# Optimization experiments

Hardware: AMD Instinct MI355X
Metric: run time of the kernel (lower is better)

## Reference

```python
import jax, jax.numpy as jnp
import numpy as np

N_NODES = 100000
N_EDGES = 600000
D = 128
BN_EPS = 1e-5


def setup_inputs() -> dict:
    key = jax.random.key(0)
    k1, k2, k3 = jax.random.split(key, 3)
    x = jax.random.normal(k1, (N_NODES, D), dtype=jnp.float32)
    edge_index = jax.random.randint(k2, (2, N_EDGES), 0, N_NODES, dtype=jnp.int64)
    # Linear(in=D, out=D): kaiming-uniform-ish init
    W = jax.random.normal(k3, (D, D), dtype=jnp.float32) / np.sqrt(D)
    b = jnp.zeros((D,), dtype=jnp.float32)
    eps_gin = jnp.zeros((), dtype=jnp.float32)  # train_eps=True, init 0
    gamma = jnp.ones((D,), dtype=jnp.float32)
    beta = jnp.zeros((D,), dtype=jnp.float32)
    return {"x": x, "edge_index": edge_index, "W": W, "b": b,
            "eps_gin": eps_gin, "gamma": gamma, "beta": beta}


def reference(x, edge_index, W, b, eps_gin, gamma, beta):
    src, dst = edge_index[0], edge_index[1]
    # GIN aggregation: sum of source features into destination nodes
    agg = jax.ops.segment_sum(x[src], dst, num_segments=N_NODES)  # [N, D]
    h = (1.0 + eps_gin) * x + agg
    # MLP([D, D]) == single Linear (PyG plain_last)
    h = jnp.einsum('nd,df->nf', h, W.T) + b  # torch Linear: h @ W^T + b
    # BatchNorm1d in training mode (batch stats, biased variance)
    mean = jnp.mean(h, axis=0)
    var = jnp.mean((h - mean) ** 2, axis=0)
    h = (h - mean) * jax.lax.rsqrt(var + BN_EPS) * gamma + beta
    h = jax.nn.relu(h)
    # residual
    return h + x
```

## Files before the change

### kernel.cpp

```cpp
#include <hip/hip_runtime.h>
#include <hip/hip_bf16.h>

#define N_NODES 100000
#define N_EDGES 600000
#define D 128
#define BN_EPS 1e-5f
#define CAP 40
#define NSLOTS 2048

typedef __bf16 bf16x8 __attribute__((ext_vector_type(8)));
typedef float floatx4 __attribute__((ext_vector_type(4)));
typedef unsigned short ushortx8 __attribute__((ext_vector_type(8)));

__device__ __forceinline__ unsigned short f2bf(float f) {
    union { float f; unsigned u; } v; v.f = f;
    unsigned u = v.u;
    unsigned r = u + 0x7FFFu + ((u >> 16) & 1u);
    return (unsigned short)(r >> 16);
}

__global__ __launch_bounds__(256) void k_fill(const int* __restrict__ ei,
                                              int* __restrict__ cursor,
                                              int* __restrict__ bucket) {
    int e = blockIdx.x * 256 + threadIdx.x;
    if (e >= N_EDGES) return;
    int src = ei[e];
    int dst = ei[N_EDGES + e];
    int pos = atomicAdd(&cursor[dst], 1);
    if (pos < CAP) bucket[dst * CAP + pos] = src;
}

__global__ __launch_bounds__(256) void k_aggregate(const float* __restrict__ x,
                                                   const int* __restrict__ cursor,
                                                   const int* __restrict__ bucket,
                                                   const float* __restrict__ epsp,
                                                   unsigned short* __restrict__ h) {
    int tid = blockIdx.x * 256 + threadIdx.x;
    int node = tid >> 5;
    if (node >= N_NODES) return;
    int lane = tid & 31;
    int deg = cursor[node];
    if (deg > CAP) deg = CAP;
    const int* bk = bucket + node * CAP;

    float4 a0 = make_float4(0.f, 0.f, 0.f, 0.f);
    float4 a1 = a0, a2 = a0, a3 = a0, a4 = a0, a5 = a0, a6 = a0, a7 = a0;

    for (int i = 0; i < deg; i += 8) {
        int rem = deg - i;
        int last = rem - 1;
        int o1 = 1 < rem ? 1 : last;
        int o2 = 2 < rem ? 2 : last;
        int o3 = 3 < rem ? 3 : last;
        int o4 = 4 < rem ? 4 : last;
        int o5 = 5 < rem ? 5 : last;
        int o6 = 6 < rem ? 6 : last;
        int o7 = 7 < rem ? 7 : last;
        int s0 = bk[i];
        int s1 = bk[i + o1];
        int s2 = bk[i + o2];
        int s3 = bk[i + o3];
        int s4 = bk[i + o4];
        int s5 = bk[i + o5];
        int s6 = bk[i + o6];
        int s7 = bk[i + o7];
        float4 v0 = ((const float4*)(x + (size_t)s0 * D))[lane];
        float4 v1 = ((const float4*)(x + (size_t)s1 * D))[lane];
        float4 v2 = ((const float4*)(x + (size_t)s2 * D))[lane];
        float4 v3 = ((const float4*)(x + (size_t)s3 * D))[lane];
        float4 v4 = ((const float4*)(x + (size_t)s4 * D))[lane];
        float4 v5 = ((const float4*)(x + (size_t)s5 * D))[lane];
        float4 v6 = ((const float4*)(x + (size_t)s6 * D))[lane];
        float4 v7 = ((const float4*)(x + (size_t)s7 * D))[lane];
        a0.x += v0.x; a0.y += v0.y; a0.z += v0.z; a0.w += v0.w;
        if (1 < rem) { a1.x += v1.x; a1.y += v1.y; a1.z += v1.z; a1.w += v1.w; }
        if (2 < rem) { a2.x += v2.x; a2.y += v2.y; a2.z += v2.z; a2.w += v2.w; }
        if (3 < rem) { a3.x += v3.x; a3.y += v3.y; a3.z += v3.z; a3.w += v3.w; }
        if (4 < rem) { a4.x += v4.x; a4.y += v4.y; a4.z += v4.z; a4.w += v4.w; }
        if (5 < rem) { a5.x += v5.x; a5.y += v5.y; a5.z += v5.z; a5.w += v5.w; }
        if (6 < rem) { a6.x += v6.x; a6.y += v6.y; a6.z += v6.z; a6.w += v6.w; }
        if (7 < rem) { a7.x += v7.x; a7.y += v7.y; a7.z += v7.z; a7.w += v7.w; }
    }
    float accx = ((a0.x + a1.x) + (a2.x + a3.x)) + ((a4.x + a5.x) + (a6.x + a7.x));
    float accy = ((a0.y + a1.y) + (a2.y + a3.y)) + ((a4.y + a5.y) + (a6.y + a7.y));
    float accz = ((a0.z + a1.z) + (a2.z + a3.z)) + ((a4.z + a5.z) + (a6.z + a7.z));
    float accw = ((a0.w + a1.w) + (a2.w + a3.w)) + ((a4.w + a5.w) + (a6.w + a7.w));

    const float one_eps = 1.0f + epsp[0];
    float4 xv = ((const float4*)(x + (size_t)node * D))[lane];
    ushort4 o;
    o.x = f2bf(one_eps * xv.x + accx);
    o.y = f2bf(one_eps * xv.y + accy);
    o.z = f2bf(one_eps * xv.z + accz);
    o.w = f2bf(one_eps * xv.w + accw);
    ((ushort4*)(h + (size_t)node * D))[lane] = o;
}

__global__ __launch_bounds__(256) void k_stats(const unsigned short* __restrict__ h,
                                               const float* __restrict__ W,
                                               float* __restrict__ pscr) {
    const int lane = threadIdx.x & 63;
    const int wid  = threadIdx.x >> 6;
    const int gw   = blockIdx.x * 4 + wid;
    const int fhalf = gw & 1;
    const int pair  = gw >> 1;
    const int npairs = gridDim.x * 2;
    const int n16  = lane & 15;
    const int quad = lane >> 4;
    const int fbase = fhalf * 64;

    bf16x8 B[4][4];
#pragma unroll
    for (int ft = 0; ft < 4; ++ft) {
#pragma unroll
        for (int ks = 0; ks < 4; ++ks) {
            const float* wp = W + (fbase + ft * 16 + n16) * D + ks * 32 + quad * 8;
            float4 wa = *(const float4*)wp;
            float4 wb = *(const float4*)(wp + 4);
            ushortx8 u;
            u[0] = f2bf(wa.x); u[1] = f2bf(wa.y); u[2] = f2bf(wa.z); u[3] = f2bf(wa.w);
            u[4] = f2bf(wb.x); u[5] = f2bf(wb.y); u[6] = f2bf(wb.z); u[7] = f2bf(wb.w);
            B[ft][ks] = __builtin_bit_cast(bf16x8, u);
        }
    }

    float psum[4] = {0.f, 0.f, 0.f, 0.f};
    float psq[4]  = {0.f, 0.f, 0.f, 0.f};

    for (int chunk = pair; chunk < N_NODES / 16; chunk += npairs) {
        const int rbase = chunk * 16;
        floatx4 acc[4];
#pragma unroll
        for (int ft = 0; ft < 4; ++ft) acc[ft] = (floatx4){0.f, 0.f, 0.f, 0.f};

#pragma unroll
        for (int ks = 0; ks < 4; ++ks) {
            const unsigned short* hp = h + (size_t)(rbase + n16) * D + ks * 32 + quad * 8;
            bf16x8 a = __builtin_bit_cast(bf16x8, *(const ushortx8*)hp);
#pragma unroll
            for (int ft = 0; ft < 4; ++ft)
                acc[ft] = __builtin_amdgcn_mfma_f32_16x16x32_bf16(a, B[ft][ks], acc[ft], 0, 0, 0);
        }

#pragma unroll
        for (int ft = 0; ft < 4; ++ft) {
#pragma unroll
            for (int i = 0; i < 4; ++i) {
                float v = acc[ft][i];
                psum[ft] += v;
                psq[ft]  += v * v;
            }
        }
    }

#pragma unroll
    for (int ft = 0; ft < 4; ++ft) {
        float s = psum[ft], q = psq[ft];
        s += __shfl_xor(s, 16, 64); q += __shfl_xor(q, 16, 64);
        s += __shfl_xor(s, 32, 64); q += __shfl_xor(q, 32, 64);
        if (quad == 0) {
            const int col = fbase + ft * 16 + n16;
            pscr[(size_t)pair * 256 + col]       = s;
            pscr[(size_t)pair * 256 + 128 + col] = q;
        }
    }
}

__global__ __launch_bounds__(256) void k_bnreduce(const float* __restrict__ pscr,
                                                  float* __restrict__ stats) {
    const int t = threadIdx.x;
    const int b = blockIdx.x;
    float acc = 0.f;
    const float* p = pscr + (size_t)b * 64 * 256 + t;
#pragma unroll 8
    for (int s = 0; s < 64; ++s)
        acc += p[(size_t)s * 256];
    unsafeAtomicAdd(&stats[t], acc);
}

__global__ __launch_bounds__(256) void k_gemm_epi(const unsigned short* __restrict__ h,
                                                  const float* __restrict__ W,
                                                  const float* __restrict__ x,
                                                  const float* __restrict__ sums,
                                                  const float* __restrict__ sumsq,
                                                  const float* __restrict__ gamma,
                                                  const float* __restrict__ beta,
                                                  float* __restrict__ out) {
    const int lane = threadIdx.x & 63;
    const int wid  = threadIdx.x >> 6;
    const int gw   = blockIdx.x * 4 + wid;
    const int fhalf = gw & 1;
    const int pair  = gw >> 1;
    const int npairs = gridDim.x * 2;
    const int n16  = lane & 15;
    const int quad = lane >> 4;
    const int fbase = fhalf * 64;

    bf16x8 B[4][4];
#pragma unroll
    for (int ft = 0; ft < 4; ++ft) {
#pragma unroll
        for (int ks = 0; ks < 4; ++ks) {
            const float* wp = W + (fbase + ft * 16 + n16) * D + ks * 32 + quad * 8;
            float4 wa = *(const float4*)wp;
            float4 wb = *(const float4*)(wp + 4);
            ushortx8 u;
            u[0] = f2bf(wa.x); u[1] = f2bf(wa.y); u[2] = f2bf(wa.z); u[3] = f2bf(wa.w);
            u[4] = f2bf(wb.x); u[5] = f2bf(wb.y); u[6] = f2bf(wb.z); u[7] = f2bf(wb.w);
            B[ft][ks] = __builtin_bit_cast(bf16x8, u);
        }
    }

    const float inv_n = 1.0f / (float)N_NODES;
    float sc[4], sh[4];
#pragma unroll
    for (int ft = 0; ft < 4; ++ft) {
        int col = fbase + ft * 16 + n16;
        float mean = sums[col] * inv_n;
        float var  = sumsq[col] * inv_n - mean * mean;
        float s    = gamma[col] * rsqrtf(var + BN_EPS);
        sc[ft] = s;
        sh[ft] = beta[col] - mean * s;
    }

    for (int chunk = pair; chunk < N_NODES / 16; chunk += npairs) {
        const int rbase = chunk * 16;
        floatx4 acc[4];
#pragma unroll
        for (int ft = 0; ft < 4; ++ft) acc[ft] = (floatx4){0.f, 0.f, 0.f, 0.f};

#pragma unroll
        for (int ks = 0; ks < 4; ++ks) {
            const unsigned short* hp = h + (size_t)(rbase + n16) * D + ks * 32 + quad * 8;
            bf16x8 a = __builtin_bit_cast(bf16x8, *(const ushortx8*)hp);
#pragma unroll
            for (int ft = 0; ft < 4; ++ft)
                acc[ft] = __builtin_amdgcn_mfma_f32_16x16x32_bf16(a, B[ft][ks], acc[ft], 0, 0, 0);
        }

#pragma unroll
        for (int ft = 0; ft < 4; ++ft) {
            const int col = fbase + ft * 16 + n16;
#pragma unroll
            for (int i = 0; i < 4; ++i) {
                const size_t idx = (size_t)(rbase + quad * 4 + i) * D + col;
                float v = acc[ft][i] * sc[ft] + sh[ft];
                v = fmaxf(v, 0.0f);
                out[idx] = v + x[idx];
            }
        }
    }
}

extern "C" void kernel_launch(void* const* d_in, const int* in_sizes, int n_in,
                              void* d_out, int out_size, void* d_ws, size_t ws_size,
                              hipStream_t stream) {
    const float* x     = (const float*)d_in[0];
    const int*   ei    = (const int*)d_in[1];
    const float* W     = (const float*)d_in[2];
    const float* epsp  = (const float*)d_in[4];
    const float* gamma = (const float*)d_in[5];
    const float* beta  = (const float*)d_in[6];
    float* out = (float*)d_out;

    char* ws = (char*)d_ws;
    int*   cursor = (int*)ws;
    float* sums   = (float*)(ws + (size_t)N_NODES * 4);
    float* sumsq  = sums + D;
    int*   bucket = (int*)(ws + (size_t)N_NODES * 4 + 2 * D * 4);
    unsigned short* h = (unsigned short*)((char*)bucket + (size_t)N_NODES * CAP * 4);
    float* pscr = (float*)bucket;

    hipMemsetAsync(cursor, 0, (size_t)N_NODES * 4 + 2 * D * 4, stream);

    k_fill<<<(N_EDGES + 255) / 256, 256, 0, stream>>>(ei, cursor, bucket);
    k_aggregate<<<(N_NODES * 32 + 255) / 256, 256, 0, stream>>>(x, cursor, bucket, epsp, h);
    k_stats<<<1024, 256, 0, stream>>>(h, W, pscr);
    k_bnreduce<<<32, 256, 0, stream>>>(pscr, sums);
    k_gemm_epi<<<1024, 256, 0, stream>>>(h, W, x, sums, sumsq, gamma, beta, out);
}
```

Measured before the change: 245.0 us.

## Gather neighbor features from a bf16 copy of x with sentinel-padded buckets

Converts x to bf16 inside the edge-fill kernel and gathers neighbor rows from that copy during aggregation, halving the bytes moved by the random gathers. Buckets are pre-filled with -1 so padding slots point at a zeroed row just before the bf16 buffer, which removes the per-slot conditional accumulation. In exchange it adds a 16MB memset, a full read and rewrite of x, and lower precision in neighbor sums. The path is only used when the workspace is large enough.

```diff
diff --git a/kernel.cpp b/kernel.cpp
--- a/kernel.cpp
+++ b/kernel.cpp
@@ -6,7 +6,6 @@
 #define D 128
 #define BN_EPS 1e-5f
 #define CAP 40
-#define NSLOTS 2048
 
 typedef __bf16 bf16x8 __attribute__((ext_vector_type(8)));
 typedef float floatx4 __attribute__((ext_vector_type(4)));
@@ -18,6 +17,87 @@
     unsigned r = u + 0x7FFFu + ((u >> 16) & 1u);
     return (unsigned short)(r >> 16);
 }
+__device__ __forceinline__ float bflo(unsigned u) {
+    union { unsigned u; float f; } v; v.u = u << 16; return v.f;
+}
+__device__ __forceinline__ float bfhi(unsigned u) {
+    union { unsigned u; float f; } v; v.u = u & 0xFFFF0000u; return v.f;
+}
+
+
+__global__ __launch_bounds__(256) void k_fill_x(const int* __restrict__ ei,
+                                                int* __restrict__ cursor,
+                                                int* __restrict__ bucket,
+                                                const float* __restrict__ x,
+                                                unsigned short* __restrict__ xb) {
+    int tid = blockIdx.x * 256 + threadIdx.x;
+    if (tid < N_EDGES) {
+        int src = ei[tid];
+        int dst = ei[N_EDGES + tid];
+        int pos = atomicAdd(&cursor[dst], 1);
+        if (pos < CAP) bucket[dst * CAP + pos] = src;
+    }
+    int c4 = tid * 4;
+    if (c4 < N_NODES * D) {
+        float4 v = *(const float4*)(x + c4);
+        ushort4 o;
+        o.x = f2bf(v.x); o.y = f2bf(v.y); o.z = f2bf(v.z); o.w = f2bf(v.w);
+        *(ushort4*)(xb + c4) = o;
+    } else {
+        unsigned j = (unsigned)(tid - N_NODES * D / 4);
+        if (j < 64) ((unsigned*)(xb - 128))[j] = 0u;
+    }
+}
+
+__global__ __launch_bounds__(256) void k_agg_bf16(const float* __restrict__ x,
+                                                  const int* __restrict__ cursor,
+                                                  const int* __restrict__ bucket,
+                                                  const unsigned short* __restrict__ xb,
+                                                  const float* __restrict__ epsp,
+                                                  unsigned short* __restrict__ h) {
+    int tid = blockIdx.x * 256 + threadIdx.x;
+    int node = tid >> 5;
+    if (node >= N_NODES) return;
+    int lane = tid & 31;
+    int deg = cursor[node];
+    if (deg > CAP) deg = CAP;
+    const int* bk = bucket + node * CAP;
+
+    float acc[8][4] = {};
+
+    for (int i = 0; i < deg; i += 8) {
+        int s[8];
+#pragma unroll
+        for (int k = 0; k < 8; ++k) s[k] = bk[i + k];
+        uint2 v[8];
+#pragma unroll
+        for (int k = 0; k < 8; ++k)
+            v[k] = ((const uint2*)(xb + (long long)s[k] * D))[lane];
+#pragma unroll
+        for (int k = 0; k < 8; ++k) {
+            acc[k][0] += bflo(v[k].x); acc[k][1] += bfhi(v[k].x);
+            acc[k][2] += bflo(v[k].y); acc[k][3] += bfhi(v[k].y);
+        }
+    }
+    float r0 = ((acc[0][0] + acc[1][0]) + (acc[2][0] + acc[3][0])) +
+               ((acc[4][0] + acc[5][0]) + (acc[6][0] + acc[7][0]));
+    float r1 = ((acc[0][1] + acc[1][1]) + (acc[2][1] + acc[3][1])) +
+               ((acc[4][1] + acc[5][1]) + (acc[6][1] + acc[7][1]));
+    float r2 = ((acc[0][2] + acc[1][2]) + (acc[2][2] + acc[3][2])) +
+               ((acc[4][2] + acc[5][2]) + (acc[6][2] + acc[7][2]));
+    float r3 = ((acc[0][3] + acc[1][3]) + (acc[2][3] + acc[3][3])) +
+               ((acc[4][3] + acc[5][3]) + (acc[6][3] + acc[7][3]));
+
+    const float one_eps = 1.0f + epsp[0];
+    float4 xv = ((const float4*)(x + (size_t)node * D))[lane];
+    ushort4 o;
+    o.x = f2bf(one_eps * xv.x + r0);
+    o.y = f2bf(one_eps * xv.y + r1);
+    o.z = f2bf(one_eps * xv.z + r2);
+    o.w = f2bf(one_eps * xv.w + r3);
+    ((ushort4*)(h + (size_t)node * D))[lane] = o;
+}
+
 
 __global__ __launch_bounds__(256) void k_fill(const int* __restrict__ ei,
                                               int* __restrict__ cursor,
@@ -96,6 +176,7 @@
     ((ushort4*)(h + (size_t)node * D))[lane] = o;
 }
 
+
 __global__ __launch_bounds__(256) void k_stats(const unsigned short* __restrict__ h,
                                                const float* __restrict__ W,
                                                float* __restrict__ pscr) {
@@ -269,12 +350,22 @@
     float* sumsq  = sums + D;
     int*   bucket = (int*)(ws + (size_t)N_NODES * 4 + 2 * D * 4);
     unsigned short* h = (unsigned short*)((char*)bucket + (size_t)N_NODES * CAP * 4);
+    unsigned short* xb = (unsigned short*)(ws + 42001280ull);
     float* pscr = (float*)bucket;
 
+    const size_t need = 42001280ull + (size_t)N_NODES * D * 2;
+
     hipMemsetAsync(cursor, 0, (size_t)N_NODES * 4 + 2 * D * 4, stream);
 
-    k_fill<<<(N_EDGES + 255) / 256, 256, 0, stream>>>(ei, cursor, bucket);
-    k_aggregate<<<(N_NODES * 32 + 255) / 256, 256, 0, stream>>>(x, cursor, bucket, epsp, h);
+    if (ws_size >= need) {
+        hipMemsetAsync(bucket, 0xFF, (size_t)N_NODES * CAP * 4, stream);
+        const int fill_threads = N_NODES * D / 4 + 64;
+        k_fill_x<<<(fill_threads + 255) / 256, 256, 0, stream>>>(ei, cursor, bucket, x, xb);
+        k_agg_bf16<<<(N_NODES * 32 + 255) / 256, 256, 0, stream>>>(x, cursor, bucket, xb, epsp, h);
+    } else {
+        k_fill<<<(N_EDGES + 255) / 256, 256, 0, stream>>>(ei, cursor, bucket);
+        k_aggregate<<<(N_NODES * 32 + 255) / 256, 256, 0, stream>>>(x, cursor, bucket, epsp, h);
+    }
     k_stats<<<1024, 256, 0, stream>>>(h, W, pscr);
     k_bnreduce<<<32, 256, 0, stream>>>(pscr, sums);
     k_gemm_epi<<<1024, 256, 0, stream>>>(h, W, x, sums, sumsq, gamma, beta, out);
```

After: 239.2 us. 2.4% less time.

## Gather bf16 copy of x in aggregation, pad atomic cursors, drop stats atomics

Applied to the files above, without the earlier changes.

Adds a bf16 copy of x, written inside the fill kernel, so the neighbour gather reads half the bytes per edge. Cursor counters are padded to one per 32 bytes when workspace allows, to cut atomic contention. The BN partial sums are now written to a buffer and reduced inside the GEMM epilogue instead of with atomics. In exchange there is an extra full pass that reads x and writes xb, and the aggregation runs at lower precision.

```diff
diff --git a/kernel.cpp b/kernel.cpp
--- a/kernel.cpp
+++ b/kernel.cpp
@@ -18,28 +18,47 @@
     unsigned r = u + 0x7FFFu + ((u >> 16) & 1u);
     return (unsigned short)(r >> 16);
 }
-
-__global__ __launch_bounds__(256) void k_fill(const int* __restrict__ ei,
-                                              int* __restrict__ cursor,
-                                              int* __restrict__ bucket) {
-    int e = blockIdx.x * 256 + threadIdx.x;
-    if (e >= N_EDGES) return;
-    int src = ei[e];
-    int dst = ei[N_EDGES + e];
-    int pos = atomicAdd(&cursor[dst], 1);
-    if (pos < CAP) bucket[dst * CAP + pos] = src;
-}
-
-__global__ __launch_bounds__(256) void k_aggregate(const float* __restrict__ x,
-                                                   const int* __restrict__ cursor,
-                                                   const int* __restrict__ bucket,
-                                                   const float* __restrict__ epsp,
-                                                   unsigned short* __restrict__ h) {
+__device__ __forceinline__ float bflo(unsigned u) {
+    union { unsigned u; float f; } v; v.u = u << 16; return v.f;
+}
+__device__ __forceinline__ float bfhi(unsigned u) {
+    union { unsigned u; float f; } v; v.u = u & 0xFFFF0000u; return v.f;
+}
+
+__global__ __launch_bounds__(256) void k_fill_x(const int* __restrict__ ei,
+                                                int* __restrict__ cursor,
+                                                int* __restrict__ bucket,
+                                                const float* __restrict__ x,
+                                                unsigned short* __restrict__ xb,
+                                                int cs) {
+    int tid = blockIdx.x * 256 + threadIdx.x;
+    if (tid < N_EDGES) {
+        int src = ei[tid];
+        int dst = ei[N_EDGES + tid];
+        int pos = atomicAdd(&cursor[dst * cs], 1);
+        if (pos < CAP) bucket[dst * CAP + pos] = src;
+    }
+    int c4 = tid * 4;
+    if (c4 < N_NODES * D) {
+        float4 v = *(const float4*)(x + c4);
+        ushort4 o;
+        o.x = f2bf(v.x); o.y = f2bf(v.y); o.z = f2bf(v.z); o.w = f2bf(v.w);
+        *(ushort4*)(xb + c4) = o;
+    }
+}
+
+__global__ __launch_bounds__(256) void k_agg_bf16(const float* __restrict__ x,
+                                                  const int* __restrict__ cursor,
+                                                  const int* __restrict__ bucket,
+                                                  const unsigned short* __restrict__ xb,
+                                                  const float* __restrict__ epsp,
+                                                  unsigned short* __restrict__ h,
+                                                  int cs) {
     int tid = blockIdx.x * 256 + threadIdx.x;
     int node = tid >> 5;
     if (node >= N_NODES) return;
     int lane = tid & 31;
-    int deg = cursor[node];
+    int deg = cursor[node * cs];
     if (deg > CAP) deg = CAP;
     const int* bk = bucket + node * CAP;
 
@@ -47,52 +66,44 @@
     float4 a1 = a0, a2 = a0, a3 = a0, a4 = a0, a5 = a0, a6 = a0, a7 = a0;
 
     for (int i = 0; i < deg; i += 8) {
-        int rem = deg - i;
-        int last = rem - 1;
-        int o1 = 1 < rem ? 1 : last;
-        int o2 = 2 < rem ? 2 : last;
-        int o3 = 3 < rem ? 3 : last;
-        int o4 = 4 < rem ? 4 : last;
-        int o5 = 5 < rem ? 5 : last;
-        int o6 = 6 < rem ? 6 : last;
-        int o7 = 7 < rem ? 7 : last;
+        int rem = deg - i, last = rem - 1;
         int s0 = bk[i];
-        int s1 = bk[i + o1];
-        int s2 = bk[i + o2];
-        int s3 = bk[i + o3];
-        int s4 = bk[i + o4];
-        int s5 = bk[i + o5];
-        int s6 = bk[i + o6];
-        int s7 = bk[i + o7];
-        float4 v0 = ((const float4*)(x + (size_t)s0 * D))[lane];
-        float4 v1 = ((const float4*)(x + (size_t)s1 * D))[lane];
-        float4 v2 = ((const float4*)(x + (size_t)s2 * D))[lane];
-        float4 v3 = ((const float4*)(x + (size_t)s3 * D))[lane];
-        float4 v4 = ((const float4*)(x + (size_t)s4 * D))[lane];
-        float4 v5 = ((const float4*)(x + (size_t)s5 * D))[lane];
-        float4 v6 = ((const float4*)(x + (size_t)s6 * D))[lane];
-        float4 v7 = ((const float4*)(x + (size_t)s7 * D))[lane];
-        a0.x += v0.x; a0.y += v0.y; a0.z += v0.z; a0.w += v0.w;
-        if (1 < rem) { a1.x += v1.x; a1.y += v1.y; a1.z += v1.z; a1.w += v1.w; }
-        if (2 < rem) { a2.x += v2.x; a2.y += v2.y; a2.z += v2.z; a2.w += v2.w; }
-        if (3 < rem) { a3.x += v3.x; a3.y += v3.y; a3.z += v3.z; a3.w += v3.w; }
-        if (4 < rem) { a4.x += v4.x; a4.y += v4.y; a4.z += v4.z; a4.w += v4.w; }
-        if (5 < rem) { a5.x += v5.x; a5.y += v5.y; a5.z += v5.z; a5.w += v5.w; }
-        if (6 < rem) { a6.x += v6.x; a6.y += v6.y; a6.z += v6.z; a6.w += v6.w; }
-        if (7 < rem) { a7.x += v7.x; a7.y += v7.y; a7.z += v7.z; a7.w += v7.w; }
-    }
-    float accx = ((a0.x + a1.x) + (a2.x + a3.x)) + ((a4.x + a5.x) + (a6.x + a7.x));
-    float accy = ((a0.y + a1.y) + (a2.y + a3.y)) + ((a4.y + a5.y) + (a6.y + a7.y));
-    float accz = ((a0.z + a1.z) + (a2.z + a3.z)) + ((a4.z + a5.z) + (a6.z + a7.z));
-    float accw = ((a0.w + a1.w) + (a2.w + a3.w)) + ((a4.w + a5.w) + (a6.w + a7.w));
+        int s1 = bk[i + (1 < rem ? 1 : last)];
+        int s2 = bk[i + (2 < rem ? 2 : last)];
+        int s3 = bk[i + (3 < rem ? 3 : last)];
+        int s4 = bk[i + (4 < rem ? 4 : last)];
+        int s5 = bk[i + (5 < rem ? 5 : last)];
+        int s6 = bk[i + (6 < rem ? 6 : last)];
+        int s7 = bk[i + (7 < rem ? 7 : last)];
+        uint2 v0 = ((const uint2*)(xb + (size_t)s0 * D))[lane];
+        uint2 v1 = ((const uint2*)(xb + (size_t)s1 * D))[lane];
+        uint2 v2 = ((const uint2*)(xb + (size_t)s2 * D))[lane];
+        uint2 v3 = ((const uint2*)(xb + (size_t)s3 * D))[lane];
+        uint2 v4 = ((const uint2*)(xb + (size_t)s4 * D))[lane];
+        uint2 v5 = ((const uint2*)(xb + (size_t)s5 * D))[lane];
+        uint2 v6 = ((const uint2*)(xb + (size_t)s6 * D))[lane];
+        uint2 v7 = ((const uint2*)(xb + (size_t)s7 * D))[lane];
+        a0.x += bflo(v0.x); a0.y += bfhi(v0.x); a0.z += bflo(v0.y); a0.w += bfhi(v0.y);
+        if (1 < rem) { a1.x += bflo(v1.x); a1.y += bfhi(v1.x); a1.z += bflo(v1.y); a1.w += bfhi(v1.y); }
+        if (2 < rem) { a2.x += bflo(v2.x); a2.y += bfhi(v2.x); a2.z += bflo(v2.y); a2.w += bfhi(v2.y); }
+        if (3 < rem) { a3.x += bflo(v3.x); a3.y += bfhi(v3.x); a3.z += bflo(v3.y); a3.w += bfhi(v3.y); }
+        if (4 < rem) { a4.x += bflo(v4.x); a4.y += bfhi(v4.x); a4.z += bflo(v4.y); a4.w += bfhi(v4.y); }
+        if (5 < rem) { a5.x += bflo(v5.x); a5.y += bfhi(v5.x); a5.z += bflo(v5.y); a5.w += bfhi(v5.y); }
+        if (6 < rem) { a6.x += bflo(v6.x); a6.y += bfhi(v6.x); a6.z += bflo(v6.y); a6.w += bfhi(v6.y); }
+        if (7 < rem) { a7.x += bflo(v7.x); a7.y += bfhi(v7.x); a7.z += bflo(v7.y); a7.w += bfhi(v7.y); }
+    }
+    float r0 = ((a0.x + a1.x) + (a2.x + a3.x)) + ((a4.x + a5.x) + (a6.x + a7.x));
+    float r1 = ((a0.y + a1.y) + (a2.y + a3.y)) + ((a4.y + a5.y) + (a6.y + a7.y));
+    float r2 = ((a0.z + a1.z) + (a2.z + a3.z)) + ((a4.z + a5.z) + (a6.z + a7.z));
+    float r3 = ((a0.w + a1.w) + (a2.w + a3.w)) + ((a4.w + a5.w) + (a6.w + a7.w));
 
     const float one_eps = 1.0f + epsp[0];
     float4 xv = ((const float4*)(x + (size_t)node * D))[lane];
     ushort4 o;
-    o.x = f2bf(one_eps * xv.x + accx);
-    o.y = f2bf(one_eps * xv.y + accy);
-    o.z = f2bf(one_eps * xv.z + accz);
-    o.w = f2bf(one_eps * xv.w + accw);
+    o.x = f2bf(one_eps * xv.x + r0);
+    o.y = f2bf(one_eps * xv.y + r1);
+    o.z = f2bf(one_eps * xv.z + r2);
+    o.w = f2bf(one_eps * xv.w + r3);
     ((ushort4*)(h + (size_t)node * D))[lane] = o;
 }
 
@@ -104,7 +115,6 @@
     const int gw   = blockIdx.x * 4 + wid;
     const int fhalf = gw & 1;
     const int pair  = gw >> 1;
-    const int npairs = gridDim.x * 2;
     const int n16  = lane & 15;
     const int quad = lane >> 4;
     const int fbase = fhalf * 64;
@@ -127,12 +137,11 @@
     float psum[4] = {0.f, 0.f, 0.f, 0.f};
     float psq[4]  = {0.f, 0.f, 0.f, 0.f};
 
-    for (int chunk = pair; chunk < N_NODES / 16; chunk += npairs) {
+    for (int chunk = pair; chunk < N_NODES / 16; chunk += NSLOTS) {
         const int rbase = chunk * 16;
         floatx4 acc[4];
 #pragma unroll
         for (int ft = 0; ft < 4; ++ft) acc[ft] = (floatx4){0.f, 0.f, 0.f, 0.f};
-
 #pragma unroll
         for (int ks = 0; ks < 4; ++ks) {
             const unsigned short* hp = h + (size_t)(rbase + n16) * D + ks * 32 + quad * 8;
@@ -141,7 +150,6 @@
             for (int ft = 0; ft < 4; ++ft)
                 acc[ft] = __builtin_amdgcn_mfma_f32_16x16x32_bf16(a, B[ft][ks], acc[ft], 0, 0, 0);
         }
-
 #pragma unroll
         for (int ft = 0; ft < 4; ++ft) {
 #pragma unroll
@@ -167,7 +175,7 @@
 }
 
 __global__ __launch_bounds__(256) void k_bnreduce(const float* __restrict__ pscr,
-                                                  float* __restrict__ stats) {
+                                                  float* __restrict__ part2) {
     const int t = threadIdx.x;
     const int b = blockIdx.x;
     float acc = 0.f;
@@ -175,14 +183,13 @@
 #pragma unroll 8
     for (int s = 0; s < 64; ++s)
         acc += p[(size_t)s * 256];
-    unsafeAtomicAdd(&stats[t], acc);
+    part2[b * 256 + t] = acc;
 }
 
 __global__ __launch_bounds__(256) void k_gemm_epi(const unsigned short* __restrict__ h,
                                                   const float* __restrict__ W,
                                                   const float* __restrict__ x,
-                                                  const float* __restrict__ sums,
-                                                  const float* __restrict__ sumsq,
+                                                  const float* __restrict__ part2,
                                                   const float* __restrict__ gamma,
                                                   const float* __restrict__ beta,
                                                   float* __restrict__ out) {
@@ -191,10 +198,19 @@
     const int gw   = blockIdx.x * 4 + wid;
     const int fhalf = gw & 1;
     const int pair  = gw >> 1;
-    const int npairs = gridDim.x * 2;
     const int n16  = lane & 15;
     const int quad = lane >> 4;
     const int fbase = fhalf * 64;
+
+    __shared__ float red[256];
+    {
+        const int t = threadIdx.x;
+        float acc = 0.f;
+#pragma unroll 8
+        for (int j = 0; j < 32; ++j)
+            acc += part2[j * 256 + t];
+        red[t] = acc;
+    }
 
     bf16x8 B[4][4];
 #pragma unroll
@@ -211,24 +227,24 @@
         }
     }
 
+    __syncthreads();
     const float inv_n = 1.0f / (float)N_NODES;
     float sc[4], sh[4];
 #pragma unroll
     for (int ft = 0; ft < 4; ++ft) {
         int col = fbase + ft * 16 + n16;
-        float mean = sums[col] * inv_n;
-        float var  = sumsq[col] * inv_n - mean * mean;
+        float mean = red[col] * inv_n;
+        float var  = red[128 + col] * inv_n - mean * mean;
         float s    = gamma[col] * rsqrtf(var + BN_EPS);
         sc[ft] = s;
         sh[ft] = beta[col] - mean * s;
     }
 
-    for (int chunk = pair; chunk < N_NODES / 16; chunk += npairs) {
+    for (int chunk = pair; chunk < N_NODES / 16; chunk += NSLOTS) {
         const int rbase = chunk * 16;
         floatx4 acc[4];
 #pragma unroll
         for (int ft = 0; ft < 4; ++ft) acc[ft] = (floatx4){0.f, 0.f, 0.f, 0.f};
-
 #pragma unroll
         for (int ks = 0; ks < 4; ++ks) {
             const unsigned short* hp = h + (size_t)(rbase + n16) * D + ks * 32 + quad * 8;
@@ -237,7 +253,6 @@
             for (int ft = 0; ft < 4; ++ft)
                 acc[ft] = __builtin_amdgcn_mfma_f32_16x16x32_bf16(a, B[ft][ks], acc[ft], 0, 0, 0);
         }
-
 #pragma unroll
         for (int ft = 0; ft < 4; ++ft) {
             const int col = fbase + ft * 16 + n16;
@@ -263,19 +278,24 @@
     const float* beta  = (const float*)d_in[6];
     float* out = (float*)d_out;
 
+    const size_t need8 = 400000ull * 8 + 16000000ull + 2 * 25600000ull;
+    const int cs = (ws_size >= need8) ? 8 : 1;
+
     char* ws = (char*)d_ws;
     int*   cursor = (int*)ws;
-    float* sums   = (float*)(ws + (size_t)N_NODES * 4);
-    float* sumsq  = sums + D;
-    int*   bucket = (int*)(ws + (size_t)N_NODES * 4 + 2 * D * 4);
-    unsigned short* h = (unsigned short*)((char*)bucket + (size_t)N_NODES * CAP * 4);
-    float* pscr = (float*)bucket;
-
-    hipMemsetAsync(cursor, 0, (size_t)N_NODES * 4 + 2 * D * 4, stream);
-
-    k_fill<<<(N_EDGES + 255) / 256, 256, 0, stream>>>(ei, cursor, bucket);
-    k_aggregate<<<(N_NODES * 32 + 255) / 256, 256, 0, stream>>>(x, cursor, bucket, epsp, h);
+    const size_t cbytes = 400000ull * cs;
+    int*   bucket = (int*)(ws + cbytes);
+    unsigned short* h  = (unsigned short*)(ws + cbytes + 16000000ull);
+    unsigned short* xb = (unsigned short*)(ws + cbytes + 16000000ull + 25600000ull);
+    float* pscr  = (float*)bucket;
+    float* part2 = (float*)ws;
+
+    hipMemsetAsync(cursor, 0, cbytes, stream);
+
+    const int fill_threads = N_NODES * D / 4;
+    k_fill_x<<<(fill_threads + 255) / 256, 256, 0, stream>>>(ei, cursor, bucket, x, xb, cs);
+    k_agg_bf16<<<(N_NODES * 32 + 255) / 256, 256, 0, stream>>>(x, cursor, bucket, xb, epsp, h, cs);
     k_stats<<<1024, 256, 0, stream>>>(h, W, pscr);
-    k_bnreduce<<<32, 256, 0, stream>>>(pscr, sums);
-    k_gemm_epi<<<1024, 256, 0, stream>>>(h, W, x, sums, sumsq, gamma, beta, out);
-}
+    k_bnreduce<<<32, 256, 0, stream>>>(pscr, part2);
+    k_gemm_epi<<<1024, 256, 0, stream>>>(h, W, x, part2, gamma, beta, out);
+}
```

Result: no change. 243.9 us (-0.5%).
